# Optimization experiments

Hardware: AMD Instinct MI355X
Metric: run time of the kernel (lower is better)

Reference implementation:

```python
import jax, jax.numpy as jnp
import numpy as np

G = 4096        # graphs
NPG = 32        # nodes per graph
N = G * NPG     # total nodes
D = 256         # hidden (inv node feat) dim
SH = 256        # shared / node-MLP hidden dim
HDG = 50        # graph head dim
HDN = 3         # node head dim
NB = 2          # num branches (dataset IDs)


def setup_inputs() -> dict:
    key = jax.random.key(0)
    ks = jax.random.split(key, 8)
    s = 0.02
    return {
        "x": jax.random.normal(ks[0], (N, D), jnp.float32),
        "dataset_name": jax.random.randint(ks[1], (G,), 0, NB, jnp.int32),
        "batch": (jnp.arange(N) // NPG).astype(jnp.int32),
        "Wgs": jax.random.normal(ks[2], (NB, D, SH), jnp.float32) * s,
        "bgs": jnp.zeros((NB, SH), jnp.float32),
        "Wgh": jax.random.normal(ks[3], (NB, SH, 2 * HDG), jnp.float32) * s,
        "bgh": jnp.zeros((NB, 2 * HDG), jnp.float32),
        "Wn1": jax.random.normal(ks[4], (NB, D, SH), jnp.float32) * s,
        "bn1": jnp.zeros((NB, SH), jnp.float32),
        "Wn2": jax.random.normal(ks[5], (NB, SH, 2 * HDN), jnp.float32) * s,
        "bn2": jnp.zeros((NB, 2 * HDN), jnp.float32),
    }


def reference(x, dataset_name, batch, Wgs, bgs, Wgh, bgh, Wn1, bn1, Wn2, bn2):
    n_nodes = x.shape[0]
    n_graphs = dataset_name.shape[0]

    # ---- graph pooling (mean) : scatter-reduce nodes -> graphs ----
    counts = jax.ops.segment_sum(jnp.ones((n_nodes,), x.dtype), batch, num_segments=n_graphs)
    x_graph = jax.ops.segment_sum(x, batch, num_segments=n_graphs) / counts[:, None]  # [G, D]

    # ---- graph head: per-branch shared MLP + head, then branch dispatch ----
    hg = jax.nn.relu(jnp.einsum("gd,bds->bgs", x_graph, Wgs) + bgs[:, None, :])       # [B, G, SH]
    og = jnp.einsum("bgs,bsh->bgh", hg, Wgh) + bgh[:, None, :]                        # [B, G, 2*HDG]
    out_g = og[dataset_name, jnp.arange(n_graphs)]                                    # [G, 2*HDG]
    g_head = out_g[:, :HDG]
    g_var = out_g[:, HDG:] ** 2

    # ---- node head (mlp type): per-branch MLP on nodes, dispatch by node's graph ID ----
    node_branch = dataset_name[batch]                                                 # [N]
    hn = jax.nn.relu(jnp.einsum("nd,bds->bns", x, Wn1) + bn1[:, None, :])             # [B, N, SH]
    on = jnp.einsum("bns,bsh->bnh", hn, Wn2) + bn2[:, None, :]                        # [B, N, 2*HDN]
    out_n = on[node_branch, jnp.arange(n_nodes)]                                      # [N, 2*HDN]
    n_head = out_n[:, :HDN]
    n_var = out_n[:, HDN:] ** 2

    # (outputs, outputs_var) flattened: heads then variance heads
    return (g_head, n_head, g_var, n_var)
```

## Files before the change

kernel.cpp:

```cpp
#include <hip/hip_runtime.h>
#include <hip/hip_bf16.h>


#define G_   4096
#define NPG_ 32
#define NN_  (G_*NPG_)
#define D_   256
#define SH_  256
#define HDG_ 50
#define HDN_ 3

#define OFF_GH 0
#define OFF_NH (G_*HDG_)
#define OFF_GV (OFF_NH + NN_*HDN_)
#define OFF_NV (OFF_GV + G_*HDG_)

typedef short v8s __attribute__((ext_vector_type(8)));
typedef short v4s __attribute__((ext_vector_type(4)));
typedef float v4f __attribute__((ext_vector_type(4)));

__device__ __forceinline__ float bfu2f(unsigned short u) {
    return __uint_as_float(((unsigned int)u) << 16);
}
__device__ __forceinline__ unsigned short f2bfu(float v) {
    __hip_bfloat16 b = __float2bfloat16(v);
    return *reinterpret_cast<unsigned short*>(&b);
}

#define MFMA16(a, b, c) __builtin_amdgcn_mfma_f32_16x16x32_bf16((a), (b), (c), 0, 0, 0)

__global__ __launch_bounds__(256) void wpack(const float* __restrict__ Wn1,
                                             const float* __restrict__ Wgs,
                                             const float* __restrict__ Wgh,
                                             const float* __restrict__ Wn2,
                                             unsigned short* __restrict__ out) {
    const int idx = blockIdx.x * 256 + threadIdx.x;
    float v;
    if (idx < 131072) {
        const int b = idx >> 16, rem = idx & 65535, s = rem >> 8, d = rem & 255;
        v = Wn1[b * 65536 + d * 256 + s];
    } else if (idx < 262144) {
        const int i2 = idx - 131072;
        const int np = i2 >> 8, d = i2 & 255;
        v = Wgs[(np >> 8) * 65536 + d * 256 + (np & 255)];
    } else if (idx < 327680) {
        const int i3 = idx - 262144;
        const int npp = i3 >> 8, k = i3 & 255;
        const int b = npp >> 7, c = npp & 127;
        v = (c < 100) ? Wgh[b * 25600 + k * 100 + c] : 0.f;
    } else {
        const int i4 = idx - 327680;
        const int b = i4 >> 12, rem = i4 & 4095, n = rem >> 8, k = rem & 255;
        v = (n < 6) ? Wn2[b * 1536 + k * 6 + n] : 0.f;
    }
    out[idx] = f2bfu(v);
}

__global__ void build_glist(const int* __restrict__ dsname,
                            int* __restrict__ glist,
                            int* __restrict__ gcnt) {
    __shared__ int cnt[2];
    const int t = threadIdx.x;
    if (t < 2) cnt[t] = 0;
    __syncthreads();
    for (int i = 0; i < 16; i++) {
        const int g = i * 256 + t;
        const int b = dsname[g];
        const int slot = atomicAdd(&cnt[b], 1);
        glist[b * G_ + slot] = g;
    }
    __syncthreads();
    if (t < 2) gcnt[t] = cnt[t];
}

__global__ __launch_bounds__(512) void node_pers(const float* __restrict__ x,
                                                 const int* __restrict__ glist,
                                                 const int* __restrict__ gcnt,
                                                 const unsigned short* __restrict__ Wn1T,
                                                 const float* __restrict__ bn1,
                                                 const unsigned short* __restrict__ Wn2b,
                                                 const float* __restrict__ bn2,
                                                 unsigned short* __restrict__ xg,
                                                 float* __restrict__ out) {
    __shared__ __align__(16) unsigned short xs[NPG_ * 264];
    __shared__ __align__(16) float red[8 * 256];
    const int t = threadIdx.x;
    const int wave = t >> 6, lane = t & 63;
    const int l15 = lane & 15, quad = lane >> 4;
    const int br = blockIdx.x & 1;
    const int bslot = blockIdx.x >> 1;
    const int cnt = gcnt[br];

    const int base_n = (wave & 1) * 128 + (wave >> 1) * 32;

    v8s B1[2][8];
    float bias1[2];
    #pragma unroll
    for (int nt = 0; nt < 2; nt++) {
        const unsigned short* bp = Wn1T + br * 65536 + (base_n + nt * 16 + l15) * 256 + quad * 8;
        #pragma unroll
        for (int kt = 0; kt < 8; kt++) B1[nt][kt] = *(const v8s*)(bp + kt * 32);
        bias1[nt] = bn1[br * 256 + base_n + nt * 16 + l15];
    }

    v8s B2[4];
    if (wave < 4) {
        const int kh = wave >> 1;
        const unsigned short* bp = Wn2b + br * 4096 + l15 * 256 + kh * 128 + quad * 8;
        #pragma unroll
        for (int j = 0; j < 4; j++) B2[j] = *(const v8s*)(bp + j * 32);
    }
    float bias2 = 0.f; int i2 = 0, c2 = 0;
    if (t < 192) { i2 = t / 6; c2 = t % 6; bias2 = bn2[br * 6 + c2]; }

    const int rb = t >> 6;
    const int colb = (t & 63) * 4;

    int gi = bslot;
    int g = glist[br * G_ + ((gi < cnt) ? gi : (cnt - 1))];
    float4 pv[4];
    #pragma unroll
    for (int k = 0; k < 4; k++)
        pv[k] = *(const float4*)(x + (size_t)g * 8192 + (rb * 4 + k) * 256 + colb);

    for (; gi < cnt; gi += 128) {
        const int gcur = g;
        float s0 = 0.f, s1 = 0.f, s2 = 0.f, s3 = 0.f;
        #pragma unroll
        for (int k = 0; k < 4; k++) {
            s0 += pv[k].x; s1 += pv[k].y; s2 += pv[k].z; s3 += pv[k].w;
            v4s bv; bv[0] = (short)f2bfu(pv[k].x); bv[1] = (short)f2bfu(pv[k].y);
                    bv[2] = (short)f2bfu(pv[k].z); bv[3] = (short)f2bfu(pv[k].w);
            *(v4s*)(&xs[(rb * 4 + k) * 264 + colb]) = bv;
        }
        *(float4*)(&red[rb * 256 + colb]) = make_float4(s0, s1, s2, s3);

        {
            const int gi2 = gi + 128;
            const int gn = glist[br * G_ + ((gi2 < cnt) ? gi2 : (cnt - 1))];
            #pragma unroll
            for (int k = 0; k < 4; k++)
                pv[k] = *(const float4*)(x + (size_t)gn * 8192 + (rb * 4 + k) * 256 + colb);
            g = gn;
        }
        __syncthreads();

        if (t < 256) {
            float m = 0.f;
            #pragma unroll
            for (int r = 0; r < 8; r++) m += red[r * 256 + t];
            xg[(size_t)gcur * 256 + t] = f2bfu(m * (1.0f / NPG_));
        }

        v4f acc[2][2];
        #pragma unroll
        for (int mt = 0; mt < 2; mt++)
            #pragma unroll
            for (int nt = 0; nt < 2; nt++) acc[mt][nt] = (v4f){0.f, 0.f, 0.f, 0.f};
        #pragma unroll
        for (int kt = 0; kt < 8; kt++) {
            const int ko = kt * 32;
            v8s a0 = *(const v8s*)(&xs[l15 * 264 + quad * 8 + ko]);
            v8s a1 = *(const v8s*)(&xs[(16 + l15) * 264 + quad * 8 + ko]);
            #pragma unroll
            for (int nt = 0; nt < 2; nt++) {
                acc[0][nt] = MFMA16(a0, B1[nt][kt], acc[0][nt]);
                acc[1][nt] = MFMA16(a1, B1[nt][kt], acc[1][nt]);
            }
        }
        __syncthreads();

        #pragma unroll
        for (int nt = 0; nt < 2; nt++) {
            const int col = base_n + nt * 16 + l15;
            #pragma unroll
            for (int mt = 0; mt < 2; mt++)
                #pragma unroll
                for (int r = 0; r < 4; r++) {
                    const int row = mt * 16 + quad * 4 + r;
                    const float v = acc[mt][nt][r] + bias1[nt];
                    xs[row * 264 + col] = f2bfu(v > 0.f ? v : 0.f);
                }
        }
        __syncthreads();

        if (wave < 4) {
            const int mtl = wave & 1, kh = wave >> 1;
            v4f a2 = (v4f){0.f, 0.f, 0.f, 0.f};
            #pragma unroll
            for (int j = 0; j < 4; j++) {
                const int ko = kh * 128 + j * 32;
                v8s av = *(const v8s*)(&xs[(mtl * 16 + l15) * 264 + ko + quad * 8]);
                a2 = MFMA16(av, B2[j], a2);
            }
            #pragma unroll
            for (int r = 0; r < 4; r++)
                red[kh * 512 + (mtl * 16 + quad * 4 + r) * 16 + l15] = a2[r];
        }
        __syncthreads();

        if (t < 192) {
            const float o = red[i2 * 16 + c2] + red[512 + i2 * 16 + c2] + bias2;
            const int n = gcur * NPG_ + i2;
            if (c2 < HDN_) out[OFF_NH + n * HDN_ + c2] = o;
            else           out[OFF_NV + n * HDN_ + (c2 - HDN_)] = o * o;
        }
        __syncthreads();
    }
}

__global__ __launch_bounds__(256) void graph_mfma2(const unsigned short* __restrict__ xg,
                                                   const int* __restrict__ dsname,
                                                   const unsigned short* __restrict__ WgsT,
                                                   const float* __restrict__ bgs,
                                                   const unsigned short* __restrict__ WghP,
                                                   const float* __restrict__ bgh,
                                                   float* __restrict__ out) {
    __shared__ __align__(16) unsigned short xs[32 * 264];
    __shared__ int bls[32];
    const int gbase = blockIdx.x * 32;
    const int t = threadIdx.x;
    const int wave = t >> 6, lane = t & 63;
    const int l15 = lane & 15, quad = lane >> 4;
    if (t < 32) bls[t] = dsname[gbase + t];

    #pragma unroll
    for (int k = 0; k < 4; k++) {
        const int flat = k * 2048 + t * 8;
        *(v8s*)(&xs[(flat >> 8) * 264 + (flat & 255)]) =
            *(const v8s*)(xg + (size_t)gbase * 256 + flat);
    }
    __syncthreads();

    v4f acc[2][8];
    #pragma unroll
    for (int mt = 0; mt < 2; mt++)
        #pragma unroll
        for (int nt = 0; nt < 8; nt++) acc[mt][nt] = (v4f){0.f, 0.f, 0.f, 0.f};

    const unsigned short* Ab = &xs[l15 * 264 + quad * 8];
    const unsigned short* Bb = WgsT + (wave * 128 + l15) * 256 + quad * 8;

    #pragma unroll
    for (int kt = 0; kt < 8; kt++) {
        const int ko = kt * 32;
        v8s a0 = *(const v8s*)(Ab + ko);
        v8s a1 = *(const v8s*)(Ab + 16 * 264 + ko);
        #pragma unroll
        for (int nt = 0; nt < 8; nt++) {
            v8s bv = *(const v8s*)(Bb + nt * 16 * 256 + ko);
            acc[0][nt] = MFMA16(a0, bv, acc[0][nt]);
            acc[1][nt] = MFMA16(a1, bv, acc[1][nt]);
        }
    }
    __syncthreads();

    {
        const int bw = wave >> 1;
        #pragma unroll
        for (int nt = 0; nt < 8; nt++) {
            const int sp = wave * 128 + nt * 16 + l15;
            const int s_local = sp & 255;
            const float bias = bgs[sp];
            #pragma unroll
            for (int mt = 0; mt < 2; mt++)
                #pragma unroll
                for (int r = 0; r < 4; r++) {
                    const int row = mt * 16 + quad * 4 + r;
                    if (bls[row] == bw) {
                        const float v = acc[mt][nt][r] + bias;
                        xs[row * 264 + s_local] = f2bfu(v > 0.f ? v : 0.f);
                    }
                }
        }
    }
    __syncthreads();

    v4f acc2[2][4];
    #pragma unroll
    for (int mt = 0; mt < 2; mt++)
        #pragma unroll
        for (int nt = 0; nt < 4; nt++) acc2[mt][nt] = (v4f){0.f, 0.f, 0.f, 0.f};

    const unsigned short* B2 = WghP + ((wave * 4) * 16 + l15) * 256 + quad * 8;
    #pragma unroll
    for (int kt = 0; kt < 8; kt++) {
        const int ko = kt * 32;
        v8s a0 = *(const v8s*)(&xs[l15 * 264 + ko + quad * 8]);
        v8s a1 = *(const v8s*)(&xs[(16 + l15) * 264 + ko + quad * 8]);
        #pragma unroll
        for (int nt = 0; nt < 4; nt++) {
            v8s bv = *(const v8s*)(B2 + nt * 16 * 256 + ko);
            acc2[0][nt] = MFMA16(a0, bv, acc2[0][nt]);
            acc2[1][nt] = MFMA16(a1, bv, acc2[1][nt]);
        }
    }

    #pragma unroll
    for (int nt = 0; nt < 4; nt++) {
        const int npp  = (wave * 4 + nt) * 16 + l15;
        const int bo   = npp >> 7, c = npp & 127;
        if (c < 2 * HDG_) {
            const float bias = bgh[bo * 2 * HDG_ + c];
            #pragma unroll
            for (int mt = 0; mt < 2; mt++)
                #pragma unroll
                for (int r = 0; r < 4; r++) {
                    const int row = mt * 16 + quad * 4 + r;
                    if (bls[row] == bo) {
                        const float o = acc2[mt][nt][r] + bias;
                        const int g = gbase + row;
                        if (c < HDG_) out[OFF_GH + g * HDG_ + c] = o;
                        else          out[OFF_GV + g * HDG_ + (c - HDG_)] = o * o;
                    }
                }
        }
    }
}

extern "C" void kernel_launch(void* const* d_in, const int* in_sizes, int n_in,
                              void* d_out, int out_size, void* d_ws, size_t ws_size,
                              hipStream_t stream) {
    const float* x      = (const float*)d_in[0];
    const int*   dsname = (const int*)d_in[1];
    const float* Wgs = (const float*)d_in[3];
    const float* bgs = (const float*)d_in[4];
    const float* Wgh = (const float*)d_in[5];
    const float* bgh = (const float*)d_in[6];
    const float* Wn1 = (const float*)d_in[7];
    const float* bn1 = (const float*)d_in[8];
    const float* Wn2 = (const float*)d_in[9];
    const float* bn2 = (const float*)d_in[10];
    float* out = (float*)d_out;

    unsigned short* wsbuf = (unsigned short*)d_ws;
    unsigned short* Wn1T  = wsbuf;
    unsigned short* WgsT  = wsbuf + 131072;
    unsigned short* WghP  = wsbuf + 262144;
    unsigned short* Wn2b  = wsbuf + 327680;
    unsigned short* xg    = wsbuf + 335872;
    int* glist = (int*)((char*)d_ws + 2768896);
    int* gcnt  = (int*)((char*)d_ws + 2801664);

    wpack      <<<1312,    256, 0, stream>>>(Wn1, Wgs, Wgh, Wn2, wsbuf);
    build_glist<<<1,       256, 0, stream>>>(dsname, glist, gcnt);
    node_pers  <<<256,     512, 0, stream>>>(x, glist, gcnt, Wn1T, bn1, Wn2b, bn2, xg, out);
    graph_mfma2<<<G_ / 32, 256, 0, stream>>>(xg, dsname, WgsT, bgs, WghP, bgh, out);
}
```

Measured before the change: 245.1 us.

## Process two graphs per node-MLP iteration and merge prep kernels

The persistent node kernel now handles a 64-row tile (two graphs) per iteration, reusing the register-resident Wn1 fragments across twice as many MFMAs. The second layer is restructured so that four waves each cover 16 rows over the full K, writing outputs directly without an LDS reduction. A separate hidden buffer removes one barrier per iteration. Weight packing and graph-list building are fused into one launch to save a kernel launch. The cost is more LDS and register pressure, and an odd graph count is padded by recomputing the last graph.

```diff
diff --git a/kernel.cpp b/kernel.cpp
--- a/kernel.cpp
+++ b/kernel.cpp
@@ -29,67 +29,71 @@
 
 #define MFMA16(a, b, c) __builtin_amdgcn_mfma_f32_16x16x32_bf16((a), (b), (c), 0, 0, 0)
 
-__global__ __launch_bounds__(256) void wpack(const float* __restrict__ Wn1,
-                                             const float* __restrict__ Wgs,
-                                             const float* __restrict__ Wgh,
-                                             const float* __restrict__ Wn2,
-                                             unsigned short* __restrict__ out) {
-    const int idx = blockIdx.x * 256 + threadIdx.x;
-    float v;
-    if (idx < 131072) {
-        const int b = idx >> 16, rem = idx & 65535, s = rem >> 8, d = rem & 255;
-        v = Wn1[b * 65536 + d * 256 + s];
-    } else if (idx < 262144) {
-        const int i2 = idx - 131072;
-        const int np = i2 >> 8, d = i2 & 255;
-        v = Wgs[(np >> 8) * 65536 + d * 256 + (np & 255)];
-    } else if (idx < 327680) {
-        const int i3 = idx - 262144;
-        const int npp = i3 >> 8, k = i3 & 255;
-        const int b = npp >> 7, c = npp & 127;
-        v = (c < 100) ? Wgh[b * 25600 + k * 100 + c] : 0.f;
+__global__ __launch_bounds__(256) void prep(const float* __restrict__ Wn1,
+                                            const float* __restrict__ Wgs,
+                                            const float* __restrict__ Wgh,
+                                            const float* __restrict__ Wn2,
+                                            unsigned short* __restrict__ wout,
+                                            const int* __restrict__ dsname,
+                                            int* __restrict__ glist,
+                                            int* __restrict__ gcnt) {
+    const int blk = blockIdx.x;
+    const int t = threadIdx.x;
+    if (blk < 1312) {
+        const int idx = blk * 256 + t;
+        float v;
+        if (idx < 131072) {
+            const int b = idx >> 16, rem = idx & 65535, s = rem >> 8, d = rem & 255;
+            v = Wn1[b * 65536 + d * 256 + s];
+        } else if (idx < 262144) {
+            const int i2 = idx - 131072;
+            const int np = i2 >> 8, d = i2 & 255;
+            v = Wgs[(np >> 8) * 65536 + d * 256 + (np & 255)];
+        } else if (idx < 327680) {
+            const int i3 = idx - 262144;
+            const int npp = i3 >> 8, k = i3 & 255;
+            const int b = npp >> 7, c = npp & 127;
+            v = (c < 100) ? Wgh[b * 25600 + k * 100 + c] : 0.f;
+        } else {
+            const int i4 = idx - 327680;
+            const int b = i4 >> 12, rem = i4 & 4095, n = rem >> 8, k = rem & 255;
+            v = (n < 6) ? Wn2[b * 1536 + k * 6 + n] : 0.f;
+        }
+        wout[idx] = f2bfu(v);
     } else {
-        const int i4 = idx - 327680;
-        const int b = i4 >> 12, rem = i4 & 4095, n = rem >> 8, k = rem & 255;
-        v = (n < 6) ? Wn2[b * 1536 + k * 6 + n] : 0.f;
-    }
-    out[idx] = f2bfu(v);
-}
-
-__global__ void build_glist(const int* __restrict__ dsname,
-                            int* __restrict__ glist,
-                            int* __restrict__ gcnt) {
-    __shared__ int cnt[2];
-    const int t = threadIdx.x;
-    if (t < 2) cnt[t] = 0;
-    __syncthreads();
-    for (int i = 0; i < 16; i++) {
-        const int g = i * 256 + t;
-        const int b = dsname[g];
-        const int slot = atomicAdd(&cnt[b], 1);
-        glist[b * G_ + slot] = g;
-    }
-    __syncthreads();
-    if (t < 2) gcnt[t] = cnt[t];
-}
-
-__global__ __launch_bounds__(512) void node_pers(const float* __restrict__ x,
-                                                 const int* __restrict__ glist,
-                                                 const int* __restrict__ gcnt,
-                                                 const unsigned short* __restrict__ Wn1T,
-                                                 const float* __restrict__ bn1,
-                                                 const unsigned short* __restrict__ Wn2b,
-                                                 const float* __restrict__ bn2,
-                                                 unsigned short* __restrict__ xg,
-                                                 float* __restrict__ out) {
-    __shared__ __align__(16) unsigned short xs[NPG_ * 264];
-    __shared__ __align__(16) float red[8 * 256];
+        __shared__ int cnt[2];
+        if (t < 2) cnt[t] = 0;
+        __syncthreads();
+        for (int i = 0; i < 16; i++) {
+            const int g = i * 256 + t;
+            const int b = dsname[g];
+            const int slot = atomicAdd(&cnt[b], 1);
+            glist[b * G_ + slot] = g;
+        }
+        __syncthreads();
+        if (t < 2) gcnt[t] = cnt[t];
+    }
+}
+
+__global__ __launch_bounds__(512) void node_pers2(const float* __restrict__ x,
+                                                  const int* __restrict__ glist,
+                                                  const int* __restrict__ gcnt,
+                                                  const unsigned short* __restrict__ Wn1T,
+                                                  const float* __restrict__ bn1,
+                                                  const unsigned short* __restrict__ Wn2b,
+                                                  const float* __restrict__ bn2,
+                                                  unsigned short* __restrict__ xg,
+                                                  float* __restrict__ out) {
+    __shared__ __align__(16) unsigned short xs[64 * 264];
+    __shared__ __align__(16) unsigned short hs[64 * 264];
+    __shared__ __align__(16) float red[16 * 256];
     const int t = threadIdx.x;
     const int wave = t >> 6, lane = t & 63;
     const int l15 = lane & 15, quad = lane >> 4;
     const int br = blockIdx.x & 1;
     const int bslot = blockIdx.x >> 1;
     const int cnt = gcnt[br];
+    const int ntile = (cnt + 1) >> 1;
 
     const int base_n = (wave & 1) * 128 + (wave >> 1) * 32;
 
@@ -103,109 +107,133 @@
         bias1[nt] = bn1[br * 256 + base_n + nt * 16 + l15];
     }
 
-    v8s B2[4];
-    if (wave < 4) {
-        const int kh = wave >> 1;
-        const unsigned short* bp = Wn2b + br * 4096 + l15 * 256 + kh * 128 + quad * 8;
-        #pragma unroll
-        for (int j = 0; j < 4; j++) B2[j] = *(const v8s*)(bp + j * 32);
-    }
-    float bias2 = 0.f; int i2 = 0, c2 = 0;
-    if (t < 192) { i2 = t / 6; c2 = t % 6; bias2 = bn2[br * 6 + c2]; }
-
-    const int rb = t >> 6;
+    v8s B2[8];
+    {
+        const unsigned short* bp = Wn2b + br * 4096 + l15 * 256 + quad * 8;
+        #pragma unroll
+        for (int kt = 0; kt < 8; kt++) B2[kt] = *(const v8s*)(bp + kt * 32);
+    }
+    float bias2 = 0.f;
+    if (l15 < 6) bias2 = bn2[br * 6 + l15];
+
+    const int r0 = t >> 6;
     const int colb = (t & 63) * 4;
 
-    int gi = bslot;
-    int g = glist[br * G_ + ((gi < cnt) ? gi : (cnt - 1))];
-    float4 pv[4];
-    #pragma unroll
-    for (int k = 0; k < 4; k++)
-        pv[k] = *(const float4*)(x + (size_t)g * 8192 + (rb * 4 + k) * 256 + colb);
-
-    for (; gi < cnt; gi += 128) {
-        const int gcur = g;
-        float s0 = 0.f, s1 = 0.f, s2 = 0.f, s3 = 0.f;
+    float4 pv[8];
+    int ga = 0, gb = 0;
+    if (bslot < ntile) {
+        const int i0 = 2 * bslot, i1 = i0 + 1;
+        ga = glist[br * G_ + i0];
+        gb = glist[br * G_ + ((i1 < cnt) ? i1 : cnt - 1)];
+        const float* xa = x + (size_t)ga * 8192 + r0 * 256 + colb;
+        const float* xb = x + (size_t)gb * 8192 + r0 * 256 + colb;
         #pragma unroll
         for (int k = 0; k < 4; k++) {
-            s0 += pv[k].x; s1 += pv[k].y; s2 += pv[k].z; s3 += pv[k].w;
-            v4s bv; bv[0] = (short)f2bfu(pv[k].x); bv[1] = (short)f2bfu(pv[k].y);
-                    bv[2] = (short)f2bfu(pv[k].z); bv[3] = (short)f2bfu(pv[k].w);
-            *(v4s*)(&xs[(rb * 4 + k) * 264 + colb]) = bv;
-        }
-        *(float4*)(&red[rb * 256 + colb]) = make_float4(s0, s1, s2, s3);
+            pv[k]     = *(const float4*)(xa + k * 2048);
+            pv[4 + k] = *(const float4*)(xb + k * 2048);
+        }
+    }
+
+    for (int ti = bslot; ti < ntile; ti += 128) {
+        const int gA = ga, gB = gb;
+
+        float4 sa = make_float4(0.f, 0.f, 0.f, 0.f);
+        float4 sb = make_float4(0.f, 0.f, 0.f, 0.f);
+        #pragma unroll
+        for (int k = 0; k < 4; k++) {
+            const float4 va = pv[k], vb = pv[4 + k];
+            sa.x += va.x; sa.y += va.y; sa.z += va.z; sa.w += va.w;
+            sb.x += vb.x; sb.y += vb.y; sb.z += vb.z; sb.w += vb.w;
+            v4s bva, bvb;
+            bva[0] = (short)f2bfu(va.x); bva[1] = (short)f2bfu(va.y);
+            bva[2] = (short)f2bfu(va.z); bva[3] = (short)f2bfu(va.w);
+            bvb[0] = (short)f2bfu(vb.x); bvb[1] = (short)f2bfu(vb.y);
+            bvb[2] = (short)f2bfu(vb.z); bvb[3] = (short)f2bfu(vb.w);
+            *(v4s*)(&xs[(r0 + 8 * k) * 264 + colb])      = bva;
+            *(v4s*)(&xs[(32 + r0 + 8 * k) * 264 + colb]) = bvb;
+        }
+        *(float4*)(&red[r0 * 256 + colb])       = sa;
+        *(float4*)(&red[(8 + r0) * 256 + colb]) = sb;
 
         {
-            const int gi2 = gi + 128;
-            const int gn = glist[br * G_ + ((gi2 < cnt) ? gi2 : (cnt - 1))];
-            #pragma unroll
-            for (int k = 0; k < 4; k++)
-                pv[k] = *(const float4*)(x + (size_t)gn * 8192 + (rb * 4 + k) * 256 + colb);
-            g = gn;
+            const int tn = ti + 128;
+            if (tn < ntile) {
+                const int i0 = 2 * tn, i1 = i0 + 1;
+                ga = glist[br * G_ + i0];
+                gb = glist[br * G_ + ((i1 < cnt) ? i1 : cnt - 1)];
+                const float* xa = x + (size_t)ga * 8192 + r0 * 256 + colb;
+                const float* xb = x + (size_t)gb * 8192 + r0 * 256 + colb;
+                #pragma unroll
+                for (int k = 0; k < 4; k++) {
+                    pv[k]     = *(const float4*)(xa + k * 2048);
+                    pv[4 + k] = *(const float4*)(xb + k * 2048);
+                }
+            }
         }
         __syncthreads();
 
-        if (t < 256) {
+        {
+            const int g = t >> 8, c = t & 255;
             float m = 0.f;
             #pragma unroll
-            for (int r = 0; r < 8; r++) m += red[r * 256 + t];
-            xg[(size_t)gcur * 256 + t] = f2bfu(m * (1.0f / NPG_));
-        }
-
-        v4f acc[2][2];
-        #pragma unroll
-        for (int mt = 0; mt < 2; mt++)
+            for (int r = 0; r < 8; r++) m += red[(g * 8 + r) * 256 + c];
+            xg[(size_t)(g ? gB : gA) * 256 + c] = f2bfu(m * (1.0f / NPG_));
+        }
+
+        v4f acc[4][2];
+        #pragma unroll
+        for (int mt = 0; mt < 4; mt++)
             #pragma unroll
             for (int nt = 0; nt < 2; nt++) acc[mt][nt] = (v4f){0.f, 0.f, 0.f, 0.f};
         #pragma unroll
         for (int kt = 0; kt < 8; kt++) {
-            const int ko = kt * 32;
-            v8s a0 = *(const v8s*)(&xs[l15 * 264 + quad * 8 + ko]);
-            v8s a1 = *(const v8s*)(&xs[(16 + l15) * 264 + quad * 8 + ko]);
+            const int ko = kt * 32 + quad * 8;
+            v8s a0 = *(const v8s*)(&xs[(     l15) * 264 + ko]);
+            v8s a1 = *(const v8s*)(&xs[(16 + l15) * 264 + ko]);
+            v8s a2 = *(const v8s*)(&xs[(32 + l15) * 264 + ko]);
+            v8s a3 = *(const v8s*)(&xs[(48 + l15) * 264 + ko]);
             #pragma unroll
             for (int nt = 0; nt < 2; nt++) {
                 acc[0][nt] = MFMA16(a0, B1[nt][kt], acc[0][nt]);
                 acc[1][nt] = MFMA16(a1, B1[nt][kt], acc[1][nt]);
+                acc[2][nt] = MFMA16(a2, B1[nt][kt], acc[2][nt]);
+                acc[3][nt] = MFMA16(a3, B1[nt][kt], acc[3][nt]);
             }
         }
-        __syncthreads();
 
         #pragma unroll
         for (int nt = 0; nt < 2; nt++) {
             const int col = base_n + nt * 16 + l15;
             #pragma unroll
-            for (int mt = 0; mt < 2; mt++)
+            for (int mt = 0; mt < 4; mt++)
                 #pragma unroll
                 for (int r = 0; r < 4; r++) {
                     const int row = mt * 16 + quad * 4 + r;
                     const float v = acc[mt][nt][r] + bias1[nt];
-                    xs[row * 264 + col] = f2bfu(v > 0.f ? v : 0.f);
+                    hs[row * 264 + col] = f2bfu(v > 0.f ? v : 0.f);
                 }
         }
         __syncthreads();
 
         if (wave < 4) {
-            const int mtl = wave & 1, kh = wave >> 1;
             v4f a2 = (v4f){0.f, 0.f, 0.f, 0.f};
             #pragma unroll
-            for (int j = 0; j < 4; j++) {
-                const int ko = kh * 128 + j * 32;
-                v8s av = *(const v8s*)(&xs[(mtl * 16 + l15) * 264 + ko + quad * 8]);
-                a2 = MFMA16(av, B2[j], a2);
+            for (int kt = 0; kt < 8; kt++) {
+                v8s av = *(const v8s*)(&hs[(wave * 16 + l15) * 264 + kt * 32 + quad * 8]);
+                a2 = MFMA16(av, B2[kt], a2);
             }
-            #pragma unroll
-            for (int r = 0; r < 4; r++)
-                red[kh * 512 + (mtl * 16 + quad * 4 + r) * 16 + l15] = a2[r];
-        }
-        __syncthreads();
-
-        if (t < 192) {
-            const float o = red[i2 * 16 + c2] + red[512 + i2 * 16 + c2] + bias2;
-            const int n = gcur * NPG_ + i2;
-            if (c2 < HDN_) out[OFF_NH + n * HDN_ + c2] = o;
-            else           out[OFF_NV + n * HDN_ + (c2 - HDN_)] = o * o;
-        }
-        __syncthreads();
+            if (l15 < 6) {
+                #pragma unroll
+                for (int r = 0; r < 4; r++) {
+                    const int row = wave * 16 + quad * 4 + r;
+                    const int g = (row < 32) ? gA : gB;
+                    const int n = g * NPG_ + (row & 31);
+                    const float v = a2[r] + bias2;
+                    if (l15 < HDN_) out[OFF_NH + n * HDN_ + l15] = v;
+                    else            out[OFF_NV + n * HDN_ + (l15 - HDN_)] = v * v;
+                }
+            }
+        }
     }
 }
 
@@ -342,8 +370,7 @@
     int* glist = (int*)((char*)d_ws + 2768896);
     int* gcnt  = (int*)((char*)d_ws + 2801664);
 
-    wpack      <<<1312,    256, 0, stream>>>(Wn1, Wgs, Wgh, Wn2, wsbuf);
-    build_glist<<<1,       256, 0, stream>>>(dsname, glist, gcnt);
-    node_pers  <<<256,     512, 0, stream>>>(x, glist, gcnt, Wn1T, bn1, Wn2b, bn2, xg, out);
+    prep       <<<1313,    256, 0, stream>>>(Wn1, Wgs, Wgh, Wn2, wsbuf, dsname, glist, gcnt);
+    node_pers2 <<<256,     512, 0, stream>>>(x, glist, gcnt, Wn1T, bn1, Wn2b, bn2, xg, out);
     graph_mfma2<<<G_ / 32, 256, 0, stream>>>(xg, dsname, WgsT, bgs, WghP, bgh, out);
 }
```

Result: no change. 246.8 us (+0.7%).
